# Performance work log

Hardware: AMD Instinct MI355X
Metric: run time of the kernel (lower is better)

## Reference

```python
import jax, jax.numpy as jnp
import numpy as np

N, L, E = 4, 2048, 1024
HID, HEADS = 1024, 16


def setup_inputs() -> dict:
    key = jax.random.key(0)
    ks = jax.random.split(key, 9)
    s_e = 1.0 / np.sqrt(E)
    s_h = 1.0 / np.sqrt(HID)
    return {
        "X_embed": jax.random.normal(ks[0], (N, L, E), dtype=jnp.float32),
        "W_q": jax.random.normal(ks[1], (E, HID), dtype=jnp.float32) * s_e,
        "b_q": jnp.zeros((HID,), dtype=jnp.float32),
        "W_k": jax.random.normal(ks[2], (E, HID), dtype=jnp.float32) * s_e,
        "b_k": jnp.zeros((HID,), dtype=jnp.float32),
        "W_v": jax.random.normal(ks[3], (E, HID), dtype=jnp.float32) * s_e,
        "b_v": jnp.zeros((HID,), dtype=jnp.float32),
        "W_o": jax.random.normal(ks[4], (HID, HID), dtype=jnp.float32) * s_h,
        "b_o": jnp.zeros((HID,), dtype=jnp.float32),
    }


def reference(X_embed, W_q, b_q, W_k, b_k, W_v, b_v, W_o, b_o):
    n, l, _ = X_embed.shape
    d = HID // HEADS
    Q = X_embed @ W_q + b_q            # (N, L, H)
    K = X_embed @ W_k + b_k
    V = X_embed @ W_v + b_v
    # Faithful to source: plain reshape (no transpose) into (N, heads, L, d)
    Q = Q.reshape(n, HEADS, l, d)
    K = K.reshape(n, HEADS, l, d)
    V = V.reshape(n, HEADS, l, d)
    # Faithful: BOTH Q and K divided by sqrt(hidden_size) -> scores / hidden_size
    scale = 1.0 / np.sqrt(HID).astype(np.float32)
    Q = Q * scale
    K = K * scale
    scores = jnp.einsum('nhax,nhbx->nhab', Q, K)      # (N, heads, L, L)
    # Faithful: softmax over dim=2 (the query axis 'a')
    attn = jax.nn.softmax(scores, axis=2)
    # Faithful: einsum 'nell,nelx->nelx' takes the DIAGONAL of attn
    diag = jnp.diagonal(attn, axis1=2, axis2=3)       # (N, heads, L)
    out = diag[..., None] * V                         # (N, heads, L, d)
    out = out.reshape(n, l, HID)
    return out @ W_o + b_o
```

## Files before the change

### kernel.cpp

```cpp
#include <hip/hip_runtime.h>
#include <type_traits>

typedef unsigned short u16;
typedef __attribute__((ext_vector_type(8))) short short8;
typedef __attribute__((ext_vector_type(4))) float floatx4;

#define DEV __device__ __forceinline__

DEV float bf2f(u16 u) { return __uint_as_float(((unsigned)u) << 16); }
DEV u16 f2bf(float f) {
  unsigned u = __float_as_uint(f);
  u += 0x7fffu + ((u >> 16) & 1u);
  return (u16)(u >> 16);
}
DEV void unpack8(uint4 v, float* f) {
  f[0] = __uint_as_float(v.x << 16); f[1] = __uint_as_float(v.x & 0xffff0000u);
  f[2] = __uint_as_float(v.y << 16); f[3] = __uint_as_float(v.y & 0xffff0000u);
  f[4] = __uint_as_float(v.z << 16); f[5] = __uint_as_float(v.z & 0xffff0000u);
  f[6] = __uint_as_float(v.w << 16); f[7] = __uint_as_float(v.w & 0xffff0000u);
}
DEV void async16(const void* g, void* lds) {
  __builtin_amdgcn_global_load_lds((const __attribute__((address_space(1))) void*)g,
                                   (__attribute__((address_space(3))) void*)lds, 16, 0, 0);
}

__global__ __launch_bounds__(256) void k_cvt_x(const float* __restrict__ X, u16* __restrict__ Xb) {
  size_t i = ((size_t)blockIdx.x * 256 + threadIdx.x) * 8;
  float4 a = *(const float4*)(X + i);
  float4 b = *(const float4*)(X + i + 4);
  union { u16 s[8]; uint4 v; } o;
  o.s[0]=f2bf(a.x); o.s[1]=f2bf(a.y); o.s[2]=f2bf(a.z); o.s[3]=f2bf(a.w);
  o.s[4]=f2bf(b.x); o.s[5]=f2bf(b.y); o.s[6]=f2bf(b.z); o.s[7]=f2bf(b.w);
  *(uint4*)(Xb + i) = o.v;
}

__global__ __launch_bounds__(256) void k_wt(const float* __restrict__ Wq, const float* __restrict__ Wk,
                                            const float* __restrict__ Wv, const float* __restrict__ Wo,
                                            const float* __restrict__ bq, const float* __restrict__ bk,
                                            const float* __restrict__ bv,
                                            u16* __restrict__ Wqkvt, u16* __restrict__ Wot,
                                            float* __restrict__ bias3) {
  const float* src; u16* dst;
  switch (blockIdx.z) {
    case 0:  src = Wq; dst = Wqkvt;            break;
    case 1:  src = Wk; dst = Wqkvt + 1048576;  break;
    case 2:  src = Wv; dst = Wqkvt + 2097152;  break;
    default: src = Wo; dst = Wot;              break;
  }
  __shared__ float tile[32][33];
  int tx = threadIdx.x & 31, ty = threadIdx.x >> 5;
  int n0 = blockIdx.x * 32, k0 = blockIdx.y * 32;
  #pragma unroll
  for (int i = 0; i < 32; i += 8) tile[ty + i][tx] = src[(size_t)(k0 + ty + i) * 1024 + n0 + tx];
  if (blockIdx.z == 3 && blockIdx.x == 0 && blockIdx.y == 0) {
    for (int i = threadIdx.x; i < 3072; i += 256)
      bias3[i] = (i < 1024) ? bq[i] : (i < 2048 ? bk[i - 1024] : bv[i - 2048]);
  }
  __syncthreads();
  #pragma unroll
  for (int i = 0; i < 32; i += 8) dst[(size_t)(n0 + ty + i) * 1024 + k0 + tx] = f2bf(tile[tx][ty + i]);
}

template <typename OutT>
__global__ __launch_bounds__(256)
void k_gemm_bt(const u16* __restrict__ A, const u16* __restrict__ B,
               const float* __restrict__ bias, OutT* __restrict__ C,
               int M, int N, int K) {
  __shared__ __align__(16) u16 As[128 * 32];
  __shared__ __align__(16) u16 Bs[128 * 32];
  const int t = threadIdx.x;
  const int w = t >> 6, lane = t & 63;
  const int m0 = blockIdx.y << 7, n0 = blockIdx.x << 7;
  const int wr = (w >> 1) << 6, wc = (w & 1) << 6;

  floatx4 acc[4][4];
  #pragma unroll
  for (int i = 0; i < 4; ++i)
    #pragma unroll
    for (int j = 0; j < 4; ++j)
      #pragma unroll
      for (int k = 0; k < 4; ++k) acc[i][j][k] = 0.f;

  const int rowA0 = t >> 2, koff = (t & 3) << 3;
  const int rowA1 = (256 + t) >> 2;
  const int lr = lane & 15, lko = (lane >> 4) << 3;

  for (int kt = 0; kt < K; kt += 32) {
    __syncthreads();
    async16(A + (size_t)(m0 + rowA0) * K + kt + koff, &As[(w << 6) * 8]);
    async16(B + (size_t)(n0 + rowA0) * K + kt + koff, &Bs[(w << 6) * 8]);
    async16(A + (size_t)(m0 + rowA1) * K + kt + koff, &As[(256 + (w << 6)) * 8]);
    async16(B + (size_t)(n0 + rowA1) * K + kt + koff, &Bs[(256 + (w << 6)) * 8]);
    __syncthreads();
    short8 af[4], bfr[4];
    #pragma unroll
    for (int i = 0; i < 4; ++i) af[i]  = *(const short8*)&As[(wr + (i << 4) + lr) * 32 + lko];
    #pragma unroll
    for (int j = 0; j < 4; ++j) bfr[j] = *(const short8*)&Bs[(wc + (j << 4) + lr) * 32 + lko];
    #pragma unroll
    for (int i = 0; i < 4; ++i)
      #pragma unroll
      for (int j = 0; j < 4; ++j)
        acc[i][j] = __builtin_amdgcn_mfma_f32_16x16x32_bf16(af[i], bfr[j], acc[i][j], 0, 0, 0);
  }
  const int lq = (lane >> 4) << 2;
  #pragma unroll
  for (int j = 0; j < 4; ++j) {
    const int cn = n0 + wc + (j << 4) + lr;
    const float bv = bias[cn];
    #pragma unroll
    for (int i = 0; i < 4; ++i) {
      const int rm = m0 + wr + (i << 4) + lq;
      #pragma unroll
      for (int rr = 0; rr < 4; ++rr) {
        float v = acc[i][j][rr] + bv;
        if constexpr (std::is_same<OutT, u16>::value) C[(size_t)(rm + rr) * N + cn] = f2bf(v);
        else                                          C[(size_t)(rm + rr) * N + cn] = v;
      }
    }
  }
}

__global__ __launch_bounds__(256)
void k_gpart(const u16* __restrict__ QKV, float* __restrict__ Gpart, float* __restrict__ qpart) {
  const int chunk = blockIdx.x;
  const int nh = blockIdx.y;
  const int n = nh >> 4, h = nh & 15;
  const int t = threadIdx.x;
  __shared__ __align__(16) float lds[128 * 68];
  const u16* Qb = QKV + (size_t)(n * 2048 + h * 128 + chunk * 16) * 3072;
  float acc[4][4];
  #pragma unroll
  for (int i = 0; i < 4; ++i)
    #pragma unroll
    for (int j = 0; j < 4; ++j) acc[i][j] = 0.f;
  float qacc[8];
  #pragma unroll
  for (int k = 0; k < 8; ++k) qacc[k] = 0.f;
  const int tx = t & 15, ty = t >> 4;
  for (int s = 0; s < 2; ++s) {
    __syncthreads();
    #pragma unroll
    for (int i = 0; i < 4; ++i) {
      int f = ((i << 8) + t) << 3;
      int row = f >> 10, j = f & 1023;
      uint4 v = *(const uint4*)(Qb + (size_t)((s << 3) + row) * 3072 + j);
      float tmp[8]; unpack8(v, tmp);
      #pragma unroll
      for (int k = 0; k < 8; ++k) qacc[k] += tmp[k];
      float* d = &lds[((row << 4) + (j >> 6)) * 68 + (j & 63)];
      #pragma unroll
      for (int k = 0; k < 8; ++k) d[k] = tmp[k];
    }
    __syncthreads();
    #pragma unroll 2
    for (int a = 0; a < 128; ++a) {
      const floatx4 qx = *(const floatx4*)&lds[a * 68 + (tx << 2)];
      const floatx4 qy = *(const floatx4*)&lds[a * 68 + (ty << 2)];
      #pragma unroll
      for (int i = 0; i < 4; ++i)
        #pragma unroll
        for (int j = 0; j < 4; ++j) acc[i][j] += qx[i] * qy[j];
    }
  }
  float* o = Gpart + ((size_t)nh * 8 + chunk) * 4096;
  #pragma unroll
  for (int i = 0; i < 4; ++i)
    #pragma unroll
    for (int j = 0; j < 4; ++j) o[((tx << 2) + i) * 64 + (ty << 2) + j] = acc[i][j];
  __syncthreads();
  #pragma unroll
  for (int k = 0; k < 8; ++k) lds[t * 8 + k] = qacc[k];
  __syncthreads();
  if (t < 64) {
    float s = 0.f;
    #pragma unroll
    for (int g = 0; g < 32; ++g) s += lds[(((t >> 3) + (g << 3)) << 3) + (t & 7)];
    qpart[((size_t)nh * 8 + chunk) * 64 + t] = s;
  }
}

__global__ __launch_bounds__(256)
void k_kgd(const u16* __restrict__ QKV, const float* __restrict__ Gpart,
           const float* __restrict__ qpart, u16* __restrict__ mid) {
  const int chunk = blockIdx.x;
  const int nh = blockIdx.y;
  const int n = nh >> 4, h = nh & 15;
  const int t = threadIdx.x, w = t >> 6, lane = t & 63;
  const int lr = lane & 15, lko = (lane >> 4) << 3;

  __shared__ u16 Gs[4096];
  __shared__ __align__(16) u16 Us[256 * 72];
  __shared__ float qs[64];

  const float* gp0 = Gpart + (size_t)nh * 8 * 4096;
  #pragma unroll
  for (int i = 0; i < 16; ++i) {
    int e = (i << 8) + t;
    float s = 0.f;
    #pragma unroll
    for (int c = 0; c < 8; ++c) s += gp0[c * 4096 + e];
    Gs[e] = f2bf(s);
  }
  if (t < 64) {
    float s = 0.f;
    #pragma unroll
    for (int rc = 0; rc < 8; ++rc) s += qpart[((size_t)nh * 8 + rc) * 64 + t];
    qs[t] = s;
  }
  __syncthreads();

  short8 af[4][2], bfr[4][2];
  #pragma unroll
  for (int i = 0; i < 4; ++i) {
    const int arow = chunk * 16 + (w << 2) + i;
    const u16* kp = QKV + (size_t)(n * 2048 + h * 128 + arow) * 3072 + 1024 + lr * 64;
    #pragma unroll
    for (int s = 0; s < 2; ++s) af[i][s] = *(const short8*)(kp + s * 32 + lko);
  }
  #pragma unroll
  for (int j = 0; j < 4; ++j)
    #pragma unroll
    for (int s = 0; s < 2; ++s)
      bfr[j][s] = *(const short8*)&Gs[((j << 4) + lr) * 64 + s * 32 + lko];
  floatx4 acc[4][4];
  #pragma unroll
  for (int i = 0; i < 4; ++i)
    #pragma unroll
    for (int j = 0; j < 4; ++j)
      #pragma unroll
      for (int k = 0; k < 4; ++k) acc[i][j][k] = 0.f;
  #pragma unroll
  for (int s = 0; s < 2; ++s)
    #pragma unroll
    for (int i = 0; i < 4; ++i)
      #pragma unroll
      for (int j = 0; j < 4; ++j)
        acc[i][j] = __builtin_amdgcn_mfma_f32_16x16x32_bf16(af[i][s], bfr[j][s], acc[i][j], 0, 0, 0);
  const int rq = (lane >> 4) << 2;
  #pragma unroll
  for (int i = 0; i < 4; ++i)
    #pragma unroll
    for (int j = 0; j < 4; ++j)
      #pragma unroll
      for (int r = 0; r < 4; ++r) {
        int a_local = (w << 6) + (i << 4) + rq + r;
        Us[a_local * 72 + (j << 4) + lr] = f2bf(acc[i][j][r]);
      }
  __syncthreads();

  const int b = chunk * 256 + t;
  const int R = n * 2048 + h * 128 + (b >> 4);
  const u16* row = QKV + (size_t)R * 3072 + ((b & 15) << 6);
  const uint4* qp = (const uint4*)row;
  const uint4* kp = (const uint4*)(row + 1024);
  const uint4* vp = (const uint4*)(row + 2048);
  const uint4* up = (const uint4*)&Us[t * 72];
  float sbb = 0.f, s1 = 0.f, quad = 0.f;
  #pragma unroll
  for (int xo = 0; xo < 8; ++xo) {
    float kx[8], qx[8], ux[8];
    unpack8(kp[xo], kx); unpack8(qp[xo], qx); unpack8(up[xo], ux);
    #pragma unroll
    for (int xi = 0; xi < 8; ++xi) {
      sbb  += qx[xi] * kx[xi];
      quad += ux[xi] * kx[xi];
      s1   += qs[xo * 8 + xi] * kx[xi];
    }
  }
  const float c1 = 0.0009765625f;
  float denom = 2048.f + s1 * c1 + 0.5f * quad * c1 * c1;
  float d = expf(sbb * c1) / denom;
  u16* mp = mid + (size_t)R * 1024 + ((b & 15) << 6);
  #pragma unroll
  for (int xo = 0; xo < 8; ++xo) {
    float f[8]; unpack8(vp[xo], f);
    union { u16 s[8]; uint4 v; } o;
    #pragma unroll
    for (int k = 0; k < 8; ++k) o.s[k] = f2bf(f[k] * d);
    *(uint4*)(mp + xo * 8) = o.v;
  }
}

extern "C" void kernel_launch(void* const* d_in, const int* in_sizes, int n_in,
                              void* d_out, int out_size, void* d_ws, size_t ws_size,
                              hipStream_t stream) {
  (void)in_sizes; (void)n_in; (void)out_size; (void)ws_size;
  const float* X  = (const float*)d_in[0];
  const float* Wq = (const float*)d_in[1];
  const float* bq = (const float*)d_in[2];
  const float* Wk = (const float*)d_in[3];
  const float* bk = (const float*)d_in[4];
  const float* Wv = (const float*)d_in[5];
  const float* bv = (const float*)d_in[6];
  const float* Wo = (const float*)d_in[7];
  const float* bo = (const float*)d_in[8];
  float* out = (float*)d_out;
  char* ws = (char*)d_ws;

  u16*   Xb    = (u16*)(ws + 0);
  u16*   mid   = (u16*)(ws + 0);
  u16*   Wqkvt = (u16*)(ws + 16777216);
  u16*   Wot   = (u16*)(ws + 23068672);
  float* bias3 = (float*)(ws + 25165824);
  u16*   QKV   = (u16*)(ws + 25182208);
  float* Gpart = (float*)(ws + 75513856);
  float* qpart = (float*)(ws + 83902464);

  k_cvt_x<<<4096, 256, 0, stream>>>(X, Xb);
  k_wt<<<dim3(32, 32, 4), 256, 0, stream>>>(Wq, Wk, Wv, Wo, bq, bk, bv, Wqkvt, Wot, bias3);
  k_gemm_bt<u16><<<dim3(24, 64), 256, 0, stream>>>(Xb, Wqkvt, bias3, QKV, 8192, 3072, 1024);
  k_gpart<<<dim3(8, 64), 256, 0, stream>>>(QKV, Gpart, qpart);
  k_kgd<<<dim3(8, 64), 256, 0, stream>>>(QKV, Gpart, qpart, mid);
  k_gemm_bt<float><<<dim3(8, 64), 256, 0, stream>>>(mid, Wot, bo, out, 8192, 1024, 1024);
}
```

Before: 257.6 us.

## Merge prep kernels and compute Gram partials with bf16 MFMA

Folds the X conversion and weight-transpose kernels into one launch, which drops a kernel launch and its gap. It also rewrites the per-chunk Q^T Q Gram partial computation to run on 16x16x32 bf16 MFMA instructions instead of scalar FP32 FMAs. Q is first transposed into LDS as bf16, and the column sums are taken with a small reduction. Inputs were already bf16, so the MFMA path should keep the numerics, but the LDS transpose stores are 16-bit scattered writes that may cause bank conflicts.

```diff
diff --git a/kernel.cpp b/kernel.cpp
--- a/kernel.cpp
+++ b/kernel.cpp
@@ -24,24 +24,26 @@
                                    (__attribute__((address_space(3))) void*)lds, 16, 0, 0);
 }
 
-__global__ __launch_bounds__(256) void k_cvt_x(const float* __restrict__ X, u16* __restrict__ Xb) {
-  size_t i = ((size_t)blockIdx.x * 256 + threadIdx.x) * 8;
-  float4 a = *(const float4*)(X + i);
-  float4 b = *(const float4*)(X + i + 4);
-  union { u16 s[8]; uint4 v; } o;
-  o.s[0]=f2bf(a.x); o.s[1]=f2bf(a.y); o.s[2]=f2bf(a.z); o.s[3]=f2bf(a.w);
-  o.s[4]=f2bf(b.x); o.s[5]=f2bf(b.y); o.s[6]=f2bf(b.z); o.s[7]=f2bf(b.w);
-  *(uint4*)(Xb + i) = o.v;
-}
-
-__global__ __launch_bounds__(256) void k_wt(const float* __restrict__ Wq, const float* __restrict__ Wk,
-                                            const float* __restrict__ Wv, const float* __restrict__ Wo,
-                                            const float* __restrict__ bq, const float* __restrict__ bk,
-                                            const float* __restrict__ bv,
-                                            u16* __restrict__ Wqkvt, u16* __restrict__ Wot,
-                                            float* __restrict__ bias3) {
+__global__ __launch_bounds__(256)
+void k_prep(const float* __restrict__ X, const float* __restrict__ Wq, const float* __restrict__ Wk,
+            const float* __restrict__ Wv, const float* __restrict__ Wo,
+            const float* __restrict__ bq, const float* __restrict__ bk, const float* __restrict__ bv,
+            u16* __restrict__ Xb, u16* __restrict__ Wqkvt, u16* __restrict__ Wot,
+            float* __restrict__ bias3) {
+  if (blockIdx.x < 4096) {
+    size_t i = ((size_t)blockIdx.x * 256 + threadIdx.x) * 8;
+    float4 a = *(const float4*)(X + i);
+    float4 b = *(const float4*)(X + i + 4);
+    union { u16 s[8]; uint4 v; } o;
+    o.s[0]=f2bf(a.x); o.s[1]=f2bf(a.y); o.s[2]=f2bf(a.z); o.s[3]=f2bf(a.w);
+    o.s[4]=f2bf(b.x); o.s[5]=f2bf(b.y); o.s[6]=f2bf(b.z); o.s[7]=f2bf(b.w);
+    *(uint4*)(Xb + i) = o.v;
+    return;
+  }
+  const int rb = blockIdx.x - 4096;
+  const int z = rb >> 10, bxx = rb & 31, byy = (rb >> 5) & 31;
   const float* src; u16* dst;
-  switch (blockIdx.z) {
+  switch (z) {
     case 0:  src = Wq; dst = Wqkvt;            break;
     case 1:  src = Wk; dst = Wqkvt + 1048576;  break;
     case 2:  src = Wv; dst = Wqkvt + 2097152;  break;
@@ -49,10 +51,10 @@
   }
   __shared__ float tile[32][33];
   int tx = threadIdx.x & 31, ty = threadIdx.x >> 5;
-  int n0 = blockIdx.x * 32, k0 = blockIdx.y * 32;
+  int n0 = bxx * 32, k0 = byy * 32;
   #pragma unroll
   for (int i = 0; i < 32; i += 8) tile[ty + i][tx] = src[(size_t)(k0 + ty + i) * 1024 + n0 + tx];
-  if (blockIdx.z == 3 && blockIdx.x == 0 && blockIdx.y == 0) {
+  if (z == 3 && bxx == 0 && byy == 0) {
     for (int i = threadIdx.x; i < 3072; i += 256)
       bias3[i] = (i < 1024) ? bq[i] : (i < 2048 ? bk[i - 1024] : bv[i - 2048]);
   }
@@ -122,62 +124,64 @@
 }
 
 __global__ __launch_bounds__(256)
-void k_gpart(const u16* __restrict__ QKV, float* __restrict__ Gpart, float* __restrict__ qpart) {
+void k_gpart2(const u16* __restrict__ QKV, float* __restrict__ Gpart, float* __restrict__ qpart) {
   const int chunk = blockIdx.x;
   const int nh = blockIdx.y;
   const int n = nh >> 4, h = nh & 15;
-  const int t = threadIdx.x;
-  __shared__ __align__(16) float lds[128 * 68];
-  const u16* Qb = QKV + (size_t)(n * 2048 + h * 128 + chunk * 16) * 3072;
-  float acc[4][4];
-  #pragma unroll
-  for (int i = 0; i < 4; ++i)
-    #pragma unroll
-    for (int j = 0; j < 4; ++j) acc[i][j] = 0.f;
-  float qacc[8];
-  #pragma unroll
-  for (int k = 0; k < 8; ++k) qacc[k] = 0.f;
-  const int tx = t & 15, ty = t >> 4;
-  for (int s = 0; s < 2; ++s) {
-    __syncthreads();
-    #pragma unroll
-    for (int i = 0; i < 4; ++i) {
-      int f = ((i << 8) + t) << 3;
-      int row = f >> 10, j = f & 1023;
-      uint4 v = *(const uint4*)(Qb + (size_t)((s << 3) + row) * 3072 + j);
-      float tmp[8]; unpack8(v, tmp);
-      #pragma unroll
-      for (int k = 0; k < 8; ++k) qacc[k] += tmp[k];
-      float* d = &lds[((row << 4) + (j >> 6)) * 68 + (j & 63)];
-      #pragma unroll
-      for (int k = 0; k < 8; ++k) d[k] = tmp[k];
+  const int t = threadIdx.x, w = t >> 6, lane = t & 63;
+  const int lr = lane & 15, lko = (lane >> 4) << 3;
+
+  __shared__ __align__(16) u16 Qt[64 * 264];
+  __shared__ float red[256];
+
+  const int a = chunk * 256 + t;
+  const uint4* qp = (const uint4*)(QKV + (size_t)(n * 2048 + h * 128 + (a >> 4)) * 3072 + ((t & 15) << 6));
+  union { u16 s[8]; uint4 v; } qv[8];
+  #pragma unroll
+  for (int j = 0; j < 8; ++j) qv[j].v = qp[j];
+  #pragma unroll
+  for (int j = 0; j < 8; ++j)
+    #pragma unroll
+    for (int e = 0; e < 8; ++e)
+      Qt[(j * 8 + e) * 264 + t] = qv[j].s[e];
+  __syncthreads();
+
+  {
+    const int x = t & 63, c = t >> 6;
+    const u16* base = &Qt[x * 264 + c * 64];
+    float s = 0.f;
+    #pragma unroll
+    for (int k = 0; k < 8; ++k) {
+      float f[8]; unpack8(*(const uint4*)(base + k * 8), f);
+      #pragma unroll
+      for (int e = 0; e < 8; ++e) s += f[e];
     }
-    __syncthreads();
-    #pragma unroll 2
-    for (int a = 0; a < 128; ++a) {
-      const floatx4 qx = *(const floatx4*)&lds[a * 68 + (tx << 2)];
-      const floatx4 qy = *(const floatx4*)&lds[a * 68 + (ty << 2)];
-      #pragma unroll
-      for (int i = 0; i < 4; ++i)
-        #pragma unroll
-        for (int j = 0; j < 4; ++j) acc[i][j] += qx[i] * qy[j];
-    }
+    red[t] = s;
+  }
+  __syncthreads();
+  if (t < 64)
+    qpart[((size_t)nh * 8 + chunk) * 64 + t] = red[t] + red[t + 64] + red[t + 128] + red[t + 192];
+
+  floatx4 acc[4];
+  #pragma unroll
+  for (int j = 0; j < 4; ++j)
+    #pragma unroll
+    for (int k = 0; k < 4; ++k) acc[j][k] = 0.f;
+  for (int ks = 0; ks < 8; ++ks) {
+    short8 f[4];
+    #pragma unroll
+    for (int i = 0; i < 4; ++i) f[i] = *(const short8*)&Qt[((i << 4) + lr) * 264 + (ks << 5) + lko];
+    #pragma unroll
+    for (int j = 0; j < 4; ++j)
+      acc[j] = __builtin_amdgcn_mfma_f32_16x16x32_bf16(f[w], f[j], acc[j], 0, 0, 0);
   }
   float* o = Gpart + ((size_t)nh * 8 + chunk) * 4096;
-  #pragma unroll
-  for (int i = 0; i < 4; ++i)
-    #pragma unroll
-    for (int j = 0; j < 4; ++j) o[((tx << 2) + i) * 64 + (ty << 2) + j] = acc[i][j];
-  __syncthreads();
-  #pragma unroll
-  for (int k = 0; k < 8; ++k) lds[t * 8 + k] = qacc[k];
-  __syncthreads();
-  if (t < 64) {
-    float s = 0.f;
-    #pragma unroll
-    for (int g = 0; g < 32; ++g) s += lds[(((t >> 3) + (g << 3)) << 3) + (t & 7)];
-    qpart[((size_t)nh * 8 + chunk) * 64 + t] = s;
-  }
+  const int quad = lane >> 4;
+  #pragma unroll
+  for (int j = 0; j < 4; ++j)
+    #pragma unroll
+    for (int r = 0; r < 4; ++r)
+      o[((w << 4) + (quad << 2) + r) * 64 + (j << 4) + lr] = acc[j][r];
 }
 
 __global__ __launch_bounds__(256)
@@ -307,10 +311,9 @@
   float* Gpart = (float*)(ws + 75513856);
   float* qpart = (float*)(ws + 83902464);
 
-  k_cvt_x<<<4096, 256, 0, stream>>>(X, Xb);
-  k_wt<<<dim3(32, 32, 4), 256, 0, stream>>>(Wq, Wk, Wv, Wo, bq, bk, bv, Wqkvt, Wot, bias3);
+  k_prep<<<8192, 256, 0, stream>>>(X, Wq, Wk, Wv, Wo, bq, bk, bv, Xb, Wqkvt, Wot, bias3);
   k_gemm_bt<u16><<<dim3(24, 64), 256, 0, stream>>>(Xb, Wqkvt, bias3, QKV, 8192, 3072, 1024);
-  k_gpart<<<dim3(8, 64), 256, 0, stream>>>(QKV, Gpart, qpart);
+  k_gpart2<<<dim3(8, 64), 256, 0, stream>>>(QKV, Gpart, qpart);
   k_kgd<<<dim3(8, 64), 256, 0, stream>>>(QKV, Gpart, qpart, mid);
   k_gemm_bt<float><<<dim3(8, 64), 256, 0, stream>>>(mid, Wot, bo, out, 8192, 1024, 1024);
 }
```

Result: slower. 263.7 us (+2.4%).
